# Kernel optimization log

Hardware: AMD Instinct MI355X
Metric: run time of the kernel (lower is better)

The kernel has to match this reference:

```python
import jax, jax.numpy as jnp
import numpy as np

H = 12      # num_heads
DIN = 768   # input_embedding_dim
D = 64      # embedding_dim (per head)
N, T = 4, 1024


def setup_inputs() -> dict:
    key = jax.random.key(0)
    ks = jax.random.split(key, 6)
    s_in = 1.0 / np.sqrt(DIN)
    s_hd = 1.0 / np.sqrt(H * D)
    x = jax.random.normal(ks[0], (N, T, DIN), dtype=jnp.float32)
    # Per-head bias-free projections stacked over heads: [H, DIN, D]
    Wq = jax.random.uniform(ks[1], (H, DIN, D), jnp.float32, -s_in, s_in)
    Wk = jax.random.uniform(ks[2], (H, DIN, D), jnp.float32, -s_in, s_in)
    Wv = jax.random.uniform(ks[3], (H, DIN, D), jnp.float32, -s_in, s_in)
    # Output projection: Linear(H*D -> D) with bias
    Wo = jax.random.uniform(ks[4], (H * D, D), jnp.float32, -s_hd, s_hd)
    bo = jax.random.uniform(ks[5], (D,), jnp.float32, -s_hd, s_hd)
    return {"x": x, "Wq": Wq, "Wk": Wk, "Wv": Wv, "Wo": Wo, "bo": bo}


def reference(x, Wq, Wk, Wv, Wo, bo):
    n, t, _ = x.shape
    # Batched per-head projections (all heads at once): [N,H,T,D]
    q = jnp.einsum('ntd,hde->nhte', x, Wq)
    k = jnp.einsum('ntd,hde->nhte', x, Wk)
    v = jnp.einsum('ntd,hde->nhte', x, Wv)
    # Raw scores (note: original applies NO 1/sqrt(D) scaling): [N,H,T,T]
    att = jnp.einsum('nhte,nhse->nhts', q, k)
    # Faithful to torch: tril zeros the upper triangle, then ALL zeros -> -inf
    causal = jnp.tril(jnp.ones((t, t), dtype=bool))
    att = jnp.where(causal, att, 0.0)
    att = jnp.where(att == 0.0, -jnp.inf, att)
    attn = jax.nn.softmax(att, axis=-1)  # [N,H,T,T]
    # Weighted values, then concat heads along feature dim (head-major order)
    o = jnp.einsum('nhts,nhse->nhte', attn, v)          # [N,H,T,D]
    o = jnp.transpose(o, (0, 2, 1, 3)).reshape(n, t, -1)  # [N,T,H*D]
    out = o @ Wo + bo  # [N,T,D]
    return out, attn
```

## Files before the change

### kernel.cpp

```cpp
#include <hip/hip_runtime.h>
#include <hip/hip_bf16.h>

typedef __hip_bfloat16 bf16;
typedef __attribute__((ext_vector_type(8))) short bf16x8;
typedef __attribute__((ext_vector_type(4))) float f32x4;

constexpr int NB  = 4;
constexpr int NH  = 12;
constexpr int SEQ = 1024;
constexpr int HD  = 64;
constexpr int DM  = 768;
constexpr int LDA = 40;

__device__ __forceinline__ bf16x8 ld8(const bf16* p){ return *(const bf16x8*)p; }
__device__ __forceinline__ f32x4 mfma16(bf16x8 a, bf16x8 b, f32x4 c){
  return __builtin_amdgcn_mfma_f32_16x16x32_bf16(a, b, c, 0, 0, 0);
}
union U8 { bf16x8 v; bf16 h[8]; };

__global__ __launch_bounds__(256) void wprep(const float* __restrict__ Wq, const float* __restrict__ Wk,
                      const float* __restrict__ Wv, const float* __restrict__ Wo,
                      bf16* __restrict__ WqTh, bf16* __restrict__ WqTl,
                      bf16* __restrict__ WkTh, bf16* __restrict__ WkTl,
                      bf16* __restrict__ WvT,  bf16* __restrict__ WoT){
  __shared__ float sT[64][65];
  const int tid = threadIdx.x;
  const int dt = blockIdx.x, y = blockIdx.y;
  const float* src; bf16* dh; bf16* dl = nullptr;
  if (y < 36){
    int z = y / 12, h = y % 12;
    src = (z==0 ? Wq : z==1 ? Wk : Wv) + (size_t)h*DM*HD;
    dh  = (z==0 ? WqTh : z==1 ? WkTh : WvT) + (size_t)h*HD*DM;
    if (z==0) dl = WqTl + (size_t)h*HD*DM;
    if (z==1) dl = WkTl + (size_t)h*HD*DM;
  } else { src = Wo; dh = WoT; }

  {
    int r = tid >> 2, c = (tid & 3) * 16;
    const float* sp = src + ((size_t)(dt*64 + r))*HD + c;
    f32x4 v0 = *(const f32x4*)sp, v1 = *(const f32x4*)(sp+4),
          v2 = *(const f32x4*)(sp+8), v3 = *(const f32x4*)(sp+12);
    #pragma unroll
    for (int j = 0; j < 4; j++){
      sT[r][c+j] = v0[j]; sT[r][c+4+j] = v1[j]; sT[r][c+8+j] = v2[j]; sT[r][c+12+j] = v3[j];
    }
  }
  __syncthreads();
  {
    int e = tid >> 2, co = (tid & 3) * 16;
    U8 uh0, ul0, uh1, ul1;
    #pragma unroll
    for (int j = 0; j < 8; j++){
      float v = sT[co + j][e];
      bf16 hi = __float2bfloat16(v);
      uh0.h[j] = hi; ul0.h[j] = __float2bfloat16(v - __bfloat162float(hi));
    }
    #pragma unroll
    for (int j = 0; j < 8; j++){
      float v = sT[co + 8 + j][e];
      bf16 hi = __float2bfloat16(v);
      uh1.h[j] = hi; ul1.h[j] = __float2bfloat16(v - __bfloat162float(hi));
    }
    size_t o = (size_t)e*DM + dt*64 + co;
    *(bf16x8*)(dh + o) = uh0.v; *(bf16x8*)(dh + o + 8) = uh1.v;
    if (dl){ *(bf16x8*)(dl + o) = ul0.v; *(bf16x8*)(dl + o + 8) = ul1.v; }
  }
}

__global__ __launch_bounds__(256) void xprep(const float* __restrict__ x,
                                             bf16* __restrict__ xh, bf16* __restrict__ xl){
  size_t base = ((size_t)blockIdx.x*256 + threadIdx.x)*8;
  f32x4 a = *(const f32x4*)(x + base), b = *(const f32x4*)(x + base + 4);
  U8 uh, ul;
  #pragma unroll
  for (int j = 0; j < 4; j++){
    bf16 h0 = __float2bfloat16(a[j]);
    uh.h[j] = h0; ul.h[j] = __float2bfloat16(a[j] - __bfloat162float(h0));
    bf16 h1 = __float2bfloat16(b[j]);
    uh.h[4+j] = h1; ul.h[4+j] = __float2bfloat16(b[j] - __bfloat162float(h1));
  }
  *(bf16x8*)(xh + base) = uh.v;
  *(bf16x8*)(xl + base) = ul.v;
}

__global__ __launch_bounds__(256) void kproj(const bf16* __restrict__ xh, const bf16* __restrict__ xl,
    const bf16* __restrict__ WqTh, const bf16* __restrict__ WqTl,
    const bf16* __restrict__ WkTh, const bf16* __restrict__ WkTl,
    const bf16* __restrict__ WvT,
    bf16* __restrict__ Qhi, bf16* __restrict__ Qlo,
    bf16* __restrict__ Khi, bf16* __restrict__ Klo, bf16* __restrict__ Vt){
  __shared__ bf16 sA[2][128*LDA];
  __shared__ bf16 sB[4][64*LDA];
  const int tid = threadIdx.x;
  const int lane = tid & 63, w = tid >> 6;
  const int quad = lane >> 4, lc = lane & 15;
  const int mb = blockIdx.x, h = blockIdx.y, z = blockIdx.z;
  const int sr = tid >> 2;
  const int sc = (tid & 3) * 8;
  const int wm = w & 1, wn = w >> 1;

  if (z == 0){
    const bf16* Bqh = WqTh + (size_t)h*HD*DM;
    const bf16* Bql = WqTl + (size_t)h*HD*DM;
    const bf16* Bkh = WkTh + (size_t)h*HD*DM;
    const bf16* Bkl = WkTl + (size_t)h*HD*DM;
    f32x4 aq[4][2] = {}, ak[4][2] = {};
    bf16x8 pa0,pa1,pa2,pa3,pq0,pq1,pk0,pk1;
    auto ldchunk = [&](int kc){
      size_t col = (size_t)kc*32 + sc;
      pa0 = ld8(xh + (size_t)(mb*128 + sr)*DM + col);
      pa1 = ld8(xh + (size_t)(mb*128 + sr + 64)*DM + col);
      pa2 = ld8(xl + (size_t)(mb*128 + sr)*DM + col);
      pa3 = ld8(xl + (size_t)(mb*128 + sr + 64)*DM + col);
      pq0 = ld8(Bqh + (size_t)sr*DM + col);
      pq1 = ld8(Bql + (size_t)sr*DM + col);
      pk0 = ld8(Bkh + (size_t)sr*DM + col);
      pk1 = ld8(Bkl + (size_t)sr*DM + col);
    };
    ldchunk(0);
    for (int kc = 0; kc < DM/32; kc++){
      *(bf16x8*)&sA[0][sr*LDA + sc] = pa0;
      *(bf16x8*)&sA[0][(sr+64)*LDA + sc] = pa1;
      *(bf16x8*)&sA[1][sr*LDA + sc] = pa2;
      *(bf16x8*)&sA[1][(sr+64)*LDA + sc] = pa3;
      *(bf16x8*)&sB[0][sr*LDA + sc] = pq0;
      *(bf16x8*)&sB[1][sr*LDA + sc] = pq1;
      *(bf16x8*)&sB[2][sr*LDA + sc] = pk0;
      *(bf16x8*)&sB[3][sr*LDA + sc] = pk1;
      __syncthreads();
      if (kc < DM/32 - 1) ldchunk(kc + 1);
      bf16x8 bqh[2], bql[2], bkh[2], bkl[2];
      #pragma unroll
      for (int nt = 0; nt < 2; nt++){
        int ro = (wn*32 + nt*16 + lc)*LDA + quad*8;
        bqh[nt] = *(const bf16x8*)&sB[0][ro];
        bql[nt] = *(const bf16x8*)&sB[1][ro];
        bkh[nt] = *(const bf16x8*)&sB[2][ro];
        bkl[nt] = *(const bf16x8*)&sB[3][ro];
      }
      #pragma unroll
      for (int mt = 0; mt < 4; mt++){
        bf16x8 ah = *(const bf16x8*)&sA[0][(wm*64 + mt*16 + lc)*LDA + quad*8];
        bf16x8 al = *(const bf16x8*)&sA[1][(wm*64 + mt*16 + lc)*LDA + quad*8];
        #pragma unroll
        for (int nt = 0; nt < 2; nt++){
          aq[mt][nt] = mfma16(ah, bqh[nt], aq[mt][nt]);
          aq[mt][nt] = mfma16(ah, bql[nt], aq[mt][nt]);
          aq[mt][nt] = mfma16(al, bqh[nt], aq[mt][nt]);
          ak[mt][nt] = mfma16(ah, bkh[nt], ak[mt][nt]);
          ak[mt][nt] = mfma16(ah, bkl[nt], ak[mt][nt]);
          ak[mt][nt] = mfma16(al, bkh[nt], ak[mt][nt]);
        }
      }
      __syncthreads();
    }
    #pragma unroll
    for (int mt = 0; mt < 4; mt++){
      #pragma unroll
      for (int nt = 0; nt < 2; nt++){
        #pragma unroll
        for (int i = 0; i < 4; i++){
          int tg = mb*128 + wm*64 + mt*16 + quad*4 + i;
          int e  = wn*32 + nt*16 + lc;
          int n = tg >> 10, t = tg & 1023;
          size_t o = ((size_t)(n*NH + h)*SEQ + t)*HD + e;
          float vq = aq[mt][nt][i];
          bf16 hq = __float2bfloat16(vq);
          Qhi[o] = hq;
          Qlo[o] = __float2bfloat16(vq - __bfloat162float(hq));
          float vk = ak[mt][nt][i];
          bf16 hk = __float2bfloat16(vk);
          Khi[o] = hk;
          Klo[o] = __float2bfloat16(vk - __bfloat162float(hk));
        }
      }
    }
  } else {
    const bf16* Av = WvT + (size_t)h*HD*DM;
    f32x4 acc[2][4] = {};
    bf16x8 pa0, pb0, pb1;
    auto ldchunk = [&](int kc){
      size_t col = (size_t)kc*32 + sc;
      pa0 = ld8(Av + (size_t)sr*DM + col);
      pb0 = ld8(xh + (size_t)(mb*128 + sr)*DM + col);
      pb1 = ld8(xh + (size_t)(mb*128 + sr + 64)*DM + col);
    };
    ldchunk(0);
    for (int kc = 0; kc < DM/32; kc++){
      *(bf16x8*)&sB[0][sr*LDA + sc] = pa0;
      *(bf16x8*)&sA[0][sr*LDA + sc] = pb0;
      *(bf16x8*)&sA[0][(sr+64)*LDA + sc] = pb1;
      __syncthreads();
      if (kc < DM/32 - 1) ldchunk(kc + 1);
      bf16x8 bt[4];
      #pragma unroll
      for (int nt = 0; nt < 4; nt++)
        bt[nt] = *(const bf16x8*)&sA[0][(wn*64 + nt*16 + lc)*LDA + quad*8];
      #pragma unroll
      for (int mt = 0; mt < 2; mt++){
        bf16x8 a = *(const bf16x8*)&sB[0][(wm*32 + mt*16 + lc)*LDA + quad*8];
        #pragma unroll
        for (int nt = 0; nt < 4; nt++)
          acc[mt][nt] = mfma16(a, bt[nt], acc[mt][nt]);
      }
      __syncthreads();
    }
    #pragma unroll
    for (int mt = 0; mt < 2; mt++){
      #pragma unroll
      for (int nt = 0; nt < 4; nt++){
        #pragma unroll
        for (int i = 0; i < 4; i++){
          int e  = wm*32 + mt*16 + quad*4 + i;
          int tg = mb*128 + wn*64 + nt*16 + lc;
          int n = tg >> 10, t = tg & 1023;
          Vt[((size_t)(n*NH + h)*HD + e)*SEQ + t] = __float2bfloat16(acc[mt][nt][i]);
        }
      }
    }
  }
}

__global__ __launch_bounds__(256) void kattn_pv(const bf16* __restrict__ Qhi, const bf16* __restrict__ Qlo,
                                                const bf16* __restrict__ Khi, const bf16* __restrict__ Klo,
                                                const bf16* __restrict__ Vt,
                                                float* __restrict__ attn, bf16* __restrict__ O){
  __shared__ bf16 sP[16][SEQ + 8];
  __shared__ float msh[4][16], lsh[4][16];
  const int tid = threadIdx.x;
  const int lane = tid & 63, w = tid >> 6;
  const int quad = lane >> 4, lc = lane & 15;
  const int lin = blockIdx.x;
  const int xcd = lin & 7;
  const int c   = lin >> 3;
  const int nh  = xcd * 6 + (c >> 6);
  const int tt  = 63 - (c & 63);
  const int t0  = tt * 16;
  const size_t base = (size_t)nh * SEQ * HD;
  const float NEGINF = -__builtin_inff();

  const int kend = t0 + 16;
  const int T_act = tt + 1;
  const int cnt   = (T_act + 3) >> 2;
  const int wbase = w * cnt;
  int wtiles = T_act - wbase;
  wtiles = wtiles < 0 ? 0 : (wtiles > cnt ? cnt : wtiles);

  f32x4 acc[16] = {};
  const bf16* qh = Qhi + base + (size_t)(t0 + lc)*HD;
  const bf16* ql = Qlo + base + (size_t)(t0 + lc)*HD;
  bf16x8 ah0 = ld8(qh + quad*8), ah1 = ld8(qh + 32 + quad*8);
  bf16x8 al0 = ld8(ql + quad*8), al1 = ld8(ql + 32 + quad*8);

  bf16x8 kb[3][4];
  auto loadK = [&](int tl, int b){
    const bf16* kh = Khi + base + (size_t)((wbase + tl)*16 + lc)*HD;
    const bf16* kl = Klo + base + (size_t)((wbase + tl)*16 + lc)*HD;
    kb[b][0] = ld8(kh + quad*8);  kb[b][1] = ld8(kh + 32 + quad*8);
    kb[b][2] = ld8(kl + quad*8);  kb[b][3] = ld8(kl + 32 + quad*8);
  };
  if (wtiles > 0) loadK(0, 0);
  if (wtiles > 1) loadK(1, 1);
  #pragma unroll
  for (int tl = 0; tl < 16; tl++){
    if (tl < wtiles){
      if (tl + 2 < wtiles) loadK(tl + 2, (tl + 2) % 3);
      const int b = tl % 3;
      acc[tl] = mfma16(ah0, kb[b][0], acc[tl]);
      acc[tl] = mfma16(ah1, kb[b][1], acc[tl]);
      acc[tl] = mfma16(ah0, kb[b][2], acc[tl]);
      acc[tl] = mfma16(ah1, kb[b][3], acc[tl]);
      acc[tl] = mfma16(al0, kb[b][0], acc[tl]);
      acc[tl] = mfma16(al1, kb[b][1], acc[tl]);
    }
  }

  float mx[4] = {NEGINF, NEGINF, NEGINF, NEGINF};
  #pragma unroll
  for (int tl = 0; tl < 16; tl++){
    if (tl < wtiles){
      int col = (wbase + tl)*16 + lc;
      #pragma unroll
      for (int i = 0; i < 4; i++){
        int r = t0 + quad*4 + i;
        float v = acc[tl][i];
        if (col <= r && v != 0.0f) mx[i] = fmaxf(mx[i], v);
      }
    }
  }
  #pragma unroll
  for (int off = 8; off; off >>= 1){
    #pragma unroll
    for (int i = 0; i < 4; i++) mx[i] = fmaxf(mx[i], __shfl_xor(mx[i], off, 16));
  }
  float sm[4] = {0.f, 0.f, 0.f, 0.f};
  #pragma unroll
  for (int tl = 0; tl < 16; tl++){
    if (tl < wtiles){
      int col = (wbase + tl)*16 + lc;
      #pragma unroll
      for (int i = 0; i < 4; i++){
        int r = t0 + quad*4 + i;
        float v = acc[tl][i];
        float e = (col <= r && v != 0.0f) ? __expf(v - mx[i]) : 0.0f;
        acc[tl][i] = e;
        sm[i] += e;
      }
    }
  }
  #pragma unroll
  for (int off = 8; off; off >>= 1){
    #pragma unroll
    for (int i = 0; i < 4; i++) sm[i] += __shfl_xor(sm[i], off, 16);
  }
  if (lc == 0){
    #pragma unroll
    for (int i = 0; i < 4; i++){ msh[w][quad*4 + i] = mx[i]; lsh[w][quad*4 + i] = sm[i]; }
  }
  __syncthreads();
  float scale[4];
  #pragma unroll
  for (int i = 0; i < 4; i++){
    int rl = quad*4 + i;
    float M = fmaxf(fmaxf(msh[0][rl], msh[1][rl]), fmaxf(msh[2][rl], msh[3][rl]));
    float L = 0.f;
    #pragma unroll
    for (int w2 = 0; w2 < 4; w2++) L += lsh[w2][rl] * __expf(msh[w2][rl] - M);
    scale[i] = __expf(mx[i] - M) / L;
  }
  #pragma unroll
  for (int tl = 0; tl < 16; tl++){
    if (tl < wtiles){
      int col = (wbase + tl)*16 + lc;
      #pragma unroll
      for (int i = 0; i < 4; i++){
        sP[quad*4 + i][col] = __float2bfloat16(acc[tl][i] * scale[i]);
      }
    }
  }
  if (kend & 31){
    sP[tid >> 4][kend + (tid & 15)] = __float2bfloat16(0.0f);
  }
  __syncthreads();

  const int colb = tid * 4;
  if (colb < kend){
    #pragma unroll
    for (int r = 0; r < 16; r++){
      const unsigned* sPu = (const unsigned*)&sP[r][0];
      uint2 v = *(const uint2*)(sPu + tid*2);
      f32x4 f;
      f[0] = __uint_as_float(v.x << 16);
      f[1] = __uint_as_float(v.x & 0xFFFF0000u);
      f[2] = __uint_as_float(v.y << 16);
      f[3] = __uint_as_float(v.y & 0xFFFF0000u);
      __builtin_nontemporal_store(f, (f32x4*)(attn + ((size_t)nh*SEQ + t0 + r)*SEQ + colb));
    }
  }

  {
    f32x4 o0 = {}, o1 = {};
    const bf16* Vb = Vt + ((size_t)nh*HD + w*16 + lc)*SEQ;
    const int nch = (kend + 31) >> 5;
    bf16x8 v0, v1, v2, v3;
    v0 = ld8(Vb + quad*8);
    if (nch > 1) v1 = ld8(Vb + 32 + quad*8);
    if (nch > 2) v2 = ld8(Vb + 64 + quad*8);
    if (nch > 3) v3 = ld8(Vb + 96 + quad*8);
    int ch = 0;
    for (; ch + 4 <= nch; ch += 4){
      const int s0 = ch*32;
      o0 = mfma16(*(const bf16x8*)&sP[lc][s0      + quad*8], v0, o0);
      if (ch + 4 < nch) v0 = ld8(Vb + (ch+4)*32 + quad*8);
      o1 = mfma16(*(const bf16x8*)&sP[lc][s0 + 32 + quad*8], v1, o1);
      if (ch + 5 < nch) v1 = ld8(Vb + (ch+5)*32 + quad*8);
      o0 = mfma16(*(const bf16x8*)&sP[lc][s0 + 64 + quad*8], v2, o0);
      if (ch + 6 < nch) v2 = ld8(Vb + (ch+6)*32 + quad*8);
      o1 = mfma16(*(const bf16x8*)&sP[lc][s0 + 96 + quad*8], v3, o1);
      if (ch + 7 < nch) v3 = ld8(Vb + (ch+7)*32 + quad*8);
    }
    if (ch < nch){ o0 = mfma16(*(const bf16x8*)&sP[lc][ch*32 + quad*8], v0, o0); ch++; }
    if (ch < nch){ o1 = mfma16(*(const bf16x8*)&sP[lc][ch*32 + quad*8], v1, o1); ch++; }
    if (ch < nch){ o0 = mfma16(*(const bf16x8*)&sP[lc][ch*32 + quad*8], v2, o0); ch++; }
    const int n = nh / NH, h = nh % NH;
    #pragma unroll
    for (int i = 0; i < 4; i++){
      O[((size_t)n*SEQ + t0 + quad*4 + i)*DM + h*HD + w*16 + lc] = __float2bfloat16(o0[i] + o1[i]);
    }
  }
}

__global__ __launch_bounds__(256) void kout(const bf16* __restrict__ O, const bf16* __restrict__ WoT,
                                            const float* __restrict__ bo, float* __restrict__ out){
  const int lane = threadIdx.x & 63, w = threadIdx.x >> 6;
  const int quad = lane >> 4, lc = lane & 15;
  const int g = blockIdx.x * 16;
  const int n = g >> 10, tb = g & 1023;
  const bf16* Or = O + ((size_t)n*SEQ + tb + lc)*DM + quad*8;
  const bf16* Wr = WoT + (size_t)(w*16 + lc)*DM + quad*8;
  f32x4 ac0 = {}, ac1 = {};
  bf16x8 a0 = ld8(Or), b0 = ld8(Wr);
  bf16x8 a1 = ld8(Or + 32),  b1 = ld8(Wr + 32);
  bf16x8 a2 = ld8(Or + 64),  b2 = ld8(Wr + 64);
  bf16x8 a3 = ld8(Or + 96),  b3 = ld8(Wr + 96);
  #pragma unroll
  for (int gr = 0; gr < 6; gr++){
    const int k0 = gr*128;
    ac0 = mfma16(a0, b0, ac0);
    if (gr < 5){ a0 = ld8(Or + k0 + 128); b0 = ld8(Wr + k0 + 128); }
    ac1 = mfma16(a1, b1, ac1);
    if (gr < 5){ a1 = ld8(Or + k0 + 160); b1 = ld8(Wr + k0 + 160); }
    ac0 = mfma16(a2, b2, ac0);
    if (gr < 5){ a2 = ld8(Or + k0 + 192); b2 = ld8(Wr + k0 + 192); }
    ac1 = mfma16(a3, b3, ac1);
    if (gr < 5){ a3 = ld8(Or + k0 + 224); b3 = ld8(Wr + k0 + 224); }
  }
  float bias = bo[w*16 + lc];
  #pragma unroll
  for (int i = 0; i < 4; i++){
    out[((size_t)n*SEQ + tb + quad*4 + i)*HD + w*16 + lc] = ac0[i] + ac1[i] + bias;
  }
}

extern "C" void kernel_launch(void* const* d_in, const int* in_sizes, int n_in,
                              void* d_out, int out_size, void* d_ws, size_t ws_size,
                              hipStream_t stream){
  const float* x  = (const float*)d_in[0];
  const float* Wq = (const float*)d_in[1];
  const float* Wk = (const float*)d_in[2];
  const float* Wv = (const float*)d_in[3];
  const float* Wo = (const float*)d_in[4];
  const float* bo = (const float*)d_in[5];

  float* out  = (float*)d_out;
  float* attn = out + (size_t)NB*SEQ*HD;

  constexpr size_t SZ_WT  = (size_t)NH*HD*DM;
  constexpr size_t SZ_WOT = (size_t)HD*DM;
  constexpr size_t SZ_Q   = (size_t)NB*NH*SEQ*HD;
  bf16* b = (bf16*)d_ws;
  bf16* WqTh = b;  b += SZ_WT;
  bf16* WqTl = b;  b += SZ_WT;
  bf16* WkTh = b;  b += SZ_WT;
  bf16* WkTl = b;  b += SZ_WT;
  bf16* WvT  = b;  b += SZ_WT;
  bf16* WoT  = b;  b += SZ_WOT;
  bf16* xh   = b;  b += SZ_Q;
  bf16* xl   = b;  b += SZ_Q;
  bf16* Qhi  = b;  b += SZ_Q;
  bf16* Qlo  = b;  b += SZ_Q;
  bf16* Khi  = b;  b += SZ_Q;
  bf16* Klo  = b;  b += SZ_Q;
  bf16* Vt   = b;  b += SZ_Q;
  bf16* O    = xh;

  wprep<<<dim3(12, 37), 256, 0, stream>>>(Wq, Wk, Wv, Wo, WqTh, WqTl, WkTh, WkTl, WvT, WoT);
  xprep<<<dim3((int)(SZ_Q/(256*8))), 256, 0, stream>>>(x, xh, xl);
  kproj<<<dim3(NB*SEQ/128, NH, 2), 256, 0, stream>>>(xh, xl, WqTh, WqTl, WkTh, WkTl, WvT,
                                                     Qhi, Qlo, Khi, Klo, Vt);
  kattn_pv<<<dim3(NB*NH*SEQ/16), 256, 0, stream>>>(Qhi, Qlo, Khi, Klo, Vt, attn, O);
  kout<<<dim3(NB*SEQ/16), 256, 0, stream>>>(O, WoT, bo, out);
}
```

Measured before the change: 336.8 us.

## Process 32 query rows per attention block with half-width shared P staging

The attention kernel now handles two 16-row query tiles per block, so each loaded K tile and V chunk is reused across 32 rows, and the grid is halved. The shared probability buffer is cut to a 512-column window processed in two passes with extra barriers, which keeps LDS use low enough for the two-blocks-per-CU launch bound. The cost is doubled accumulator registers and extra synchronisation per pass; the K prefetch depth also drops from two tiles ahead to one.

```diff
diff --git a/kernel.cpp b/kernel.cpp
--- a/kernel.cpp
+++ b/kernel.cpp
@@ -221,38 +221,42 @@
   }
 }
 
-__global__ __launch_bounds__(256) void kattn_pv(const bf16* __restrict__ Qhi, const bf16* __restrict__ Qlo,
-                                                const bf16* __restrict__ Khi, const bf16* __restrict__ Klo,
-                                                const bf16* __restrict__ Vt,
-                                                float* __restrict__ attn, bf16* __restrict__ O){
-  __shared__ bf16 sP[16][SEQ + 8];
-  __shared__ float msh[4][16], lsh[4][16];
+__global__ __launch_bounds__(256, 2) void kattn_pv(const bf16* __restrict__ Qhi, const bf16* __restrict__ Qlo,
+                                                   const bf16* __restrict__ Khi, const bf16* __restrict__ Klo,
+                                                   const bf16* __restrict__ Vt,
+                                                   float* __restrict__ attn, bf16* __restrict__ O){
+  __shared__ bf16 sP[32][528];
+  __shared__ float msh[4][32], lsh[4][32];
   const int tid = threadIdx.x;
   const int lane = tid & 63, w = tid >> 6;
   const int quad = lane >> 4, lc = lane & 15;
   const int lin = blockIdx.x;
   const int xcd = lin & 7;
   const int c   = lin >> 3;
-  const int nh  = xcd * 6 + (c >> 6);
-  const int tt  = 63 - (c & 63);
-  const int t0  = tt * 16;
+  const int nh  = xcd * 6 + (c >> 5);
+  const int tp  = 31 - (c & 31);
+  const int t0  = tp * 32;
   const size_t base = (size_t)nh * SEQ * HD;
   const float NEGINF = -__builtin_inff();
 
-  const int kend = t0 + 16;
-  const int T_act = tt + 1;
+  const int kend = t0 + 32;
+  const int T_act = 2*tp + 2;
   const int cnt   = (T_act + 3) >> 2;
   const int wbase = w * cnt;
   int wtiles = T_act - wbase;
   wtiles = wtiles < 0 ? 0 : (wtiles > cnt ? cnt : wtiles);
 
-  f32x4 acc[16] = {};
-  const bf16* qh = Qhi + base + (size_t)(t0 + lc)*HD;
-  const bf16* ql = Qlo + base + (size_t)(t0 + lc)*HD;
-  bf16x8 ah0 = ld8(qh + quad*8), ah1 = ld8(qh + 32 + quad*8);
-  bf16x8 al0 = ld8(ql + quad*8), al1 = ld8(ql + 32 + quad*8);
-
-  bf16x8 kb[3][4];
+  f32x4 acc[2][16] = {};
+  bf16x8 qa[2][4];
+  #pragma unroll
+  for (int rt = 0; rt < 2; rt++){
+    const bf16* qh = Qhi + base + (size_t)(t0 + rt*16 + lc)*HD;
+    const bf16* ql = Qlo + base + (size_t)(t0 + rt*16 + lc)*HD;
+    qa[rt][0] = ld8(qh + quad*8); qa[rt][1] = ld8(qh + 32 + quad*8);
+    qa[rt][2] = ld8(ql + quad*8); qa[rt][3] = ld8(ql + 32 + quad*8);
+  }
+
+  bf16x8 kb[2][4];
   auto loadK = [&](int tl, int b){
     const bf16* kh = Khi + base + (size_t)((wbase + tl)*16 + lc)*HD;
     const bf16* kl = Klo + base + (size_t)((wbase + tl)*16 + lc)*HD;
@@ -260,133 +264,168 @@
     kb[b][2] = ld8(kl + quad*8);  kb[b][3] = ld8(kl + 32 + quad*8);
   };
   if (wtiles > 0) loadK(0, 0);
-  if (wtiles > 1) loadK(1, 1);
   #pragma unroll
   for (int tl = 0; tl < 16; tl++){
     if (tl < wtiles){
-      if (tl + 2 < wtiles) loadK(tl + 2, (tl + 2) % 3);
-      const int b = tl % 3;
-      acc[tl] = mfma16(ah0, kb[b][0], acc[tl]);
-      acc[tl] = mfma16(ah1, kb[b][1], acc[tl]);
-      acc[tl] = mfma16(ah0, kb[b][2], acc[tl]);
-      acc[tl] = mfma16(ah1, kb[b][3], acc[tl]);
-      acc[tl] = mfma16(al0, kb[b][0], acc[tl]);
-      acc[tl] = mfma16(al1, kb[b][1], acc[tl]);
-    }
-  }
-
-  float mx[4] = {NEGINF, NEGINF, NEGINF, NEGINF};
+      if (tl + 1 < wtiles) loadK(tl + 1, (tl + 1) & 1);
+      const int b = tl & 1;
+      #pragma unroll
+      for (int rt = 0; rt < 2; rt++){
+        acc[rt][tl] = mfma16(qa[rt][0], kb[b][0], acc[rt][tl]);
+        acc[rt][tl] = mfma16(qa[rt][1], kb[b][1], acc[rt][tl]);
+        acc[rt][tl] = mfma16(qa[rt][0], kb[b][2], acc[rt][tl]);
+        acc[rt][tl] = mfma16(qa[rt][1], kb[b][3], acc[rt][tl]);
+        acc[rt][tl] = mfma16(qa[rt][2], kb[b][0], acc[rt][tl]);
+        acc[rt][tl] = mfma16(qa[rt][3], kb[b][1], acc[rt][tl]);
+      }
+    }
+  }
+
+  float mx[2][4], sm[2][4];
+  #pragma unroll
+  for (int rt = 0; rt < 2; rt++)
+    #pragma unroll
+    for (int i = 0; i < 4; i++){ mx[rt][i] = NEGINF; sm[rt][i] = 0.f; }
+
   #pragma unroll
   for (int tl = 0; tl < 16; tl++){
     if (tl < wtiles){
       int col = (wbase + tl)*16 + lc;
       #pragma unroll
-      for (int i = 0; i < 4; i++){
-        int r = t0 + quad*4 + i;
-        float v = acc[tl][i];
-        if (col <= r && v != 0.0f) mx[i] = fmaxf(mx[i], v);
-      }
-    }
-  }
-  #pragma unroll
-  for (int off = 8; off; off >>= 1){
-    #pragma unroll
-    for (int i = 0; i < 4; i++) mx[i] = fmaxf(mx[i], __shfl_xor(mx[i], off, 16));
-  }
-  float sm[4] = {0.f, 0.f, 0.f, 0.f};
+      for (int rt = 0; rt < 2; rt++){
+        #pragma unroll
+        for (int i = 0; i < 4; i++){
+          int r = t0 + rt*16 + quad*4 + i;
+          float v = acc[rt][tl][i];
+          if (col <= r && v != 0.0f) mx[rt][i] = fmaxf(mx[rt][i], v);
+        }
+      }
+    }
+  }
+  #pragma unroll
+  for (int off = 8; off; off >>= 1)
+    #pragma unroll
+    for (int rt = 0; rt < 2; rt++)
+      #pragma unroll
+      for (int i = 0; i < 4; i++) mx[rt][i] = fmaxf(mx[rt][i], __shfl_xor(mx[rt][i], off, 16));
+
   #pragma unroll
   for (int tl = 0; tl < 16; tl++){
     if (tl < wtiles){
       int col = (wbase + tl)*16 + lc;
       #pragma unroll
+      for (int rt = 0; rt < 2; rt++){
+        #pragma unroll
+        for (int i = 0; i < 4; i++){
+          int r = t0 + rt*16 + quad*4 + i;
+          float v = acc[rt][tl][i];
+          float e = (col <= r && v != 0.0f) ? __expf(v - mx[rt][i]) : 0.0f;
+          acc[rt][tl][i] = e;
+          sm[rt][i] += e;
+        }
+      }
+    }
+  }
+  #pragma unroll
+  for (int off = 8; off; off >>= 1)
+    #pragma unroll
+    for (int rt = 0; rt < 2; rt++)
+      #pragma unroll
+      for (int i = 0; i < 4; i++) sm[rt][i] += __shfl_xor(sm[rt][i], off, 16);
+
+  if (lc == 0){
+    #pragma unroll
+    for (int rt = 0; rt < 2; rt++)
+      #pragma unroll
       for (int i = 0; i < 4; i++){
-        int r = t0 + quad*4 + i;
-        float v = acc[tl][i];
-        float e = (col <= r && v != 0.0f) ? __expf(v - mx[i]) : 0.0f;
-        acc[tl][i] = e;
-        sm[i] += e;
-      }
-    }
-  }
-  #pragma unroll
-  for (int off = 8; off; off >>= 1){
-    #pragma unroll
-    for (int i = 0; i < 4; i++) sm[i] += __shfl_xor(sm[i], off, 16);
-  }
-  if (lc == 0){
-    #pragma unroll
-    for (int i = 0; i < 4; i++){ msh[w][quad*4 + i] = mx[i]; lsh[w][quad*4 + i] = sm[i]; }
+        msh[w][rt*16 + quad*4 + i] = mx[rt][i];
+        lsh[w][rt*16 + quad*4 + i] = sm[rt][i];
+      }
   }
   __syncthreads();
-  float scale[4];
+  float scale[2][4];
+  #pragma unroll
+  for (int rt = 0; rt < 2; rt++){
+    #pragma unroll
+    for (int i = 0; i < 4; i++){
+      int rl = rt*16 + quad*4 + i;
+      float M = fmaxf(fmaxf(msh[0][rl], msh[1][rl]), fmaxf(msh[2][rl], msh[3][rl]));
+      float L = 0.f;
+      #pragma unroll
+      for (int w2 = 0; w2 < 4; w2++) L += lsh[w2][rl] * __expf(msh[w2][rl] - M);
+      scale[rt][i] = __expf(mx[rt][i] - M) / L;
+    }
+  }
+
+  f32x4 o0a = {}, o0b = {}, o1a = {}, o1b = {};
+  #pragma unroll
+  for (int hh = 0; hh < 2; hh++){
+    const int lo = hh * 512;
+    if (lo < kend){
+      const int hi = (kend < lo + 512) ? kend : lo + 512;
+      #pragma unroll
+      for (int tl = 0; tl < 16; tl++){
+        if (tl < wtiles && ((wbase + tl) >> 5) == hh){
+          int col = (wbase + tl)*16 + lc - lo;
+          #pragma unroll
+          for (int rt = 0; rt < 2; rt++)
+            #pragma unroll
+            for (int i = 0; i < 4; i++)
+              sP[rt*16 + quad*4 + i][col] = __float2bfloat16(acc[rt][tl][i] * scale[rt][i]);
+        }
+      }
+      __syncthreads();
+
+      {
+        const int colb = (tid & 127) * 4;
+        const int rh = tid >> 7;
+        if (colb < hi - lo){
+          #pragma unroll
+          for (int rp = 0; rp < 16; rp++){
+            int r = rp*2 + rh;
+            const unsigned* sPu = (const unsigned*)&sP[r][0];
+            uint2 v = *(const uint2*)(sPu + (tid & 127)*2);
+            f32x4 f;
+            f[0] = __uint_as_float(v.x << 16);
+            f[1] = __uint_as_float(v.x & 0xFFFF0000u);
+            f[2] = __uint_as_float(v.y << 16);
+            f[3] = __uint_as_float(v.y & 0xFFFF0000u);
+            __builtin_nontemporal_store(f, (f32x4*)(attn + ((size_t)nh*SEQ + t0 + r)*SEQ + lo + colb));
+          }
+        }
+      }
+
+      {
+        const int nch = (hi - lo) >> 5;
+        const bf16* Vb = Vt + ((size_t)nh*HD + w*16 + lc)*SEQ + lo;
+        bf16x8 v0, v1;
+        v0 = ld8(Vb + quad*8);
+        if (nch > 1) v1 = ld8(Vb + 32 + quad*8);
+        int ch = 0;
+        for (; ch + 2 <= nch; ch += 2){
+          const int s0 = ch*32;
+          o0a = mfma16(*(const bf16x8*)&sP[lc][s0 + quad*8],      v0, o0a);
+          o1a = mfma16(*(const bf16x8*)&sP[16 + lc][s0 + quad*8], v0, o1a);
+          if (ch + 2 < nch) v0 = ld8(Vb + (ch+2)*32 + quad*8);
+          o0b = mfma16(*(const bf16x8*)&sP[lc][s0 + 32 + quad*8],      v1, o0b);
+          o1b = mfma16(*(const bf16x8*)&sP[16 + lc][s0 + 32 + quad*8], v1, o1b);
+          if (ch + 3 < nch) v1 = ld8(Vb + (ch+3)*32 + quad*8);
+        }
+        if (ch < nch){
+          const int s0 = ch*32;
+          o0a = mfma16(*(const bf16x8*)&sP[lc][s0 + quad*8],      v0, o0a);
+          o1a = mfma16(*(const bf16x8*)&sP[16 + lc][s0 + quad*8], v0, o1a);
+        }
+      }
+      __syncthreads();
+    }
+  }
+
+  const int n = nh / NH, h = nh % NH;
   #pragma unroll
   for (int i = 0; i < 4; i++){
-    int rl = quad*4 + i;
-    float M = fmaxf(fmaxf(msh[0][rl], msh[1][rl]), fmaxf(msh[2][rl], msh[3][rl]));
-    float L = 0.f;
-    #pragma unroll
-    for (int w2 = 0; w2 < 4; w2++) L += lsh[w2][rl] * __expf(msh[w2][rl] - M);
-    scale[i] = __expf(mx[i] - M) / L;
-  }
-  #pragma unroll
-  for (int tl = 0; tl < 16; tl++){
-    if (tl < wtiles){
-      int col = (wbase + tl)*16 + lc;
-      #pragma unroll
-      for (int i = 0; i < 4; i++){
-        sP[quad*4 + i][col] = __float2bfloat16(acc[tl][i] * scale[i]);
-      }
-    }
-  }
-  if (kend & 31){
-    sP[tid >> 4][kend + (tid & 15)] = __float2bfloat16(0.0f);
-  }
-  __syncthreads();
-
-  const int colb = tid * 4;
-  if (colb < kend){
-    #pragma unroll
-    for (int r = 0; r < 16; r++){
-      const unsigned* sPu = (const unsigned*)&sP[r][0];
-      uint2 v = *(const uint2*)(sPu + tid*2);
-      f32x4 f;
-      f[0] = __uint_as_float(v.x << 16);
-      f[1] = __uint_as_float(v.x & 0xFFFF0000u);
-      f[2] = __uint_as_float(v.y << 16);
-      f[3] = __uint_as_float(v.y & 0xFFFF0000u);
-      __builtin_nontemporal_store(f, (f32x4*)(attn + ((size_t)nh*SEQ + t0 + r)*SEQ + colb));
-    }
-  }
-
-  {
-    f32x4 o0 = {}, o1 = {};
-    const bf16* Vb = Vt + ((size_t)nh*HD + w*16 + lc)*SEQ;
-    const int nch = (kend + 31) >> 5;
-    bf16x8 v0, v1, v2, v3;
-    v0 = ld8(Vb + quad*8);
-    if (nch > 1) v1 = ld8(Vb + 32 + quad*8);
-    if (nch > 2) v2 = ld8(Vb + 64 + quad*8);
-    if (nch > 3) v3 = ld8(Vb + 96 + quad*8);
-    int ch = 0;
-    for (; ch + 4 <= nch; ch += 4){
-      const int s0 = ch*32;
-      o0 = mfma16(*(const bf16x8*)&sP[lc][s0      + quad*8], v0, o0);
-      if (ch + 4 < nch) v0 = ld8(Vb + (ch+4)*32 + quad*8);
-      o1 = mfma16(*(const bf16x8*)&sP[lc][s0 + 32 + quad*8], v1, o1);
-      if (ch + 5 < nch) v1 = ld8(Vb + (ch+5)*32 + quad*8);
-      o0 = mfma16(*(const bf16x8*)&sP[lc][s0 + 64 + quad*8], v2, o0);
-      if (ch + 6 < nch) v2 = ld8(Vb + (ch+6)*32 + quad*8);
-      o1 = mfma16(*(const bf16x8*)&sP[lc][s0 + 96 + quad*8], v3, o1);
-      if (ch + 7 < nch) v3 = ld8(Vb + (ch+7)*32 + quad*8);
-    }
-    if (ch < nch){ o0 = mfma16(*(const bf16x8*)&sP[lc][ch*32 + quad*8], v0, o0); ch++; }
-    if (ch < nch){ o1 = mfma16(*(const bf16x8*)&sP[lc][ch*32 + quad*8], v1, o1); ch++; }
-    if (ch < nch){ o0 = mfma16(*(const bf16x8*)&sP[lc][ch*32 + quad*8], v2, o0); ch++; }
-    const int n = nh / NH, h = nh % NH;
-    #pragma unroll
-    for (int i = 0; i < 4; i++){
-      O[((size_t)n*SEQ + t0 + quad*4 + i)*DM + h*HD + w*16 + lc] = __float2bfloat16(o0[i] + o1[i]);
-    }
+    O[((size_t)n*SEQ + t0 + quad*4 + i)*DM + h*HD + w*16 + lc]      = __float2bfloat16(o0a[i] + o0b[i]);
+    O[((size_t)n*SEQ + t0 + 16 + quad*4 + i)*DM + h*HD + w*16 + lc] = __float2bfloat16(o1a[i] + o1b[i]);
   }
 }
 
@@ -458,6 +497,6 @@
   xprep<<<dim3((int)(SZ_Q/(256*8))), 256, 0, stream>>>(x, xh, xl);
   kproj<<<dim3(NB*SEQ/128, NH, 2), 256, 0, stream>>>(xh, xl, WqTh, WqTl, WkTh, WkTl, WvT,
                                                      Qhi, Qlo, Khi, Klo, Vt);
-  kattn_pv<<<dim3(NB*NH*SEQ/16), 256, 0, stream>>>(Qhi, Qlo, Khi, Klo, Vt, attn, O);
+  kattn_pv<<<dim3(NB*NH*SEQ/32), 256, 0, stream>>>(Qhi, Qlo, Khi, Klo, Vt, attn, O);
   kout<<<dim3(NB*SEQ/16), 256, 0, stream>>>(O, WoT, bo, out);
 }
```

After: 310.3 us. 7.8% less time.
